# Performance work log

Hardware: AMD Instinct MI355X
Metric: run time of the kernel (lower is better)

## Reference

```python
import jax, jax.numpy as jnp
import numpy as np

N_NODES = 100000
N_EDGES = 600000
DIM = 128
LN_EPS = 1e-5


def setup_inputs() -> dict:
    key = jax.random.key(0)
    ks = jax.random.split(key, 12)
    s = 1.0 / np.sqrt(DIM)
    return {
        "h": jax.random.normal(ks[0], (N_NODES, DIM), dtype=jnp.float32),
        "edge_src": jax.random.randint(ks[1], (N_EDGES,), 0, N_NODES, dtype=jnp.int32),
        "edge_dst": jax.random.randint(ks[2], (N_EDGES,), 0, N_NODES, dtype=jnp.int32),
        "W_self": jax.random.uniform(ks[3], (DIM, DIM), jnp.float32, -s, s),
        "b_self": jax.random.uniform(ks[4], (DIM,), jnp.float32, -s, s),
        "W_neigh": jax.random.uniform(ks[5], (DIM, DIM), jnp.float32, -s, s),
        "b_neigh": jax.random.uniform(ks[6], (DIM,), jnp.float32, -s, s),
        "W_gate": jax.random.uniform(ks[7], (DIM, 2 * DIM), jnp.float32, -s, s),
        "b_gate": jax.random.uniform(ks[8], (DIM,), jnp.float32, -s, s),
        "ln_gamma": jnp.ones((DIM,), jnp.float32),
        "ln_beta": jnp.zeros((DIM,), jnp.float32),
    }


def reference(h, edge_src, edge_dst, W_self, b_self, W_neigh, b_neigh, W_gate, b_gate, ln_gamma, ln_beta):
    n = h.shape[0]
    # self transform: [N, D]
    hs = h @ W_self.T + b_self
    # mean over predecessors via segment sum over edges (src -> dst)
    neigh_sum = jax.ops.segment_sum(h[edge_src], edge_dst, num_segments=n)
    counts = jax.ops.segment_sum(jnp.ones((edge_src.shape[0],), h.dtype), edge_dst, num_segments=n)
    has_pred = (counts > 0).astype(h.dtype)[:, None]
    neigh_mean = neigh_sum / jnp.maximum(counts, 1.0)[:, None]
    hn = neigh_mean @ W_neigh.T + b_neigh
    # nodes with no predecessors skip the neighbor term entirely (incl. bias)
    m = hs + has_pred * hn
    gate = jax.nn.sigmoid(jnp.concatenate([h, m], axis=-1) @ W_gate.T + b_gate)
    v = gate * m + (1.0 - gate) * h
    # LayerNorm (biased variance, as torch) + relu
    mu = jnp.mean(v, axis=-1, keepdims=True)
    var = jnp.mean(jnp.square(v - mu), axis=-1, keepdims=True)
    out = (v - mu) * jax.lax.rsqrt(var + LN_EPS) * ln_gamma + ln_beta
    return jax.nn.relu(out)
```

## Files before the change

### kernel.cpp

```cpp
#include <hip/hip_runtime.h>
#include <math.h>

#define N_NODES 100000
#define N_EDGES 600000
#define DIM 128
#define LN_EPS 1e-5f
#define SCAN_NBLK ((N_NODES + 255) / 256)
#define NTILES ((N_NODES + 127) / 128)
#define NODE_GRID 256

typedef __bf16 bf16x8 __attribute__((ext_vector_type(8)));
typedef __bf16 bf16x4 __attribute__((ext_vector_type(4)));
typedef float f32x4 __attribute__((ext_vector_type(4)));

__global__ __launch_bounds__(256)
void prep_kernel(const float* __restrict__ h, const int* __restrict__ edst,
                 __bf16* __restrict__ h_bf, int* __restrict__ counts) {
  int i = blockIdx.x * 256 + threadIdx.x;
  {
    const float4 v0 = *reinterpret_cast<const float4*>(h + (size_t)i * 8);
    const float4 v1 = *reinterpret_cast<const float4*>(h + (size_t)i * 8 + 4);
    bf16x8 b;
    b[0] = (__bf16)v0.x; b[1] = (__bf16)v0.y; b[2] = (__bf16)v0.z; b[3] = (__bf16)v0.w;
    b[4] = (__bf16)v1.x; b[5] = (__bf16)v1.y; b[6] = (__bf16)v1.z; b[7] = (__bf16)v1.w;
    *reinterpret_cast<bf16x8*>(h_bf + (size_t)i * 8) = b;
  }
  if (i < N_EDGES) atomicAdd(&counts[edst[i]], 1);
}

__global__ __launch_bounds__(256)
void scan1_kernel(const int* __restrict__ counts, int* __restrict__ block_sums) {
  int i = blockIdx.x * 256 + threadIdx.x;
  int v = (i < N_NODES) ? counts[i] : 0;
#pragma unroll
  for (int off = 1; off < 64; off <<= 1) v += __shfl_xor(v, off);
  __shared__ int ws[4];
  if ((threadIdx.x & 63) == 0) ws[threadIdx.x >> 6] = v;
  __syncthreads();
  if (threadIdx.x == 0) block_sums[blockIdx.x] = ws[0] + ws[1] + ws[2] + ws[3];
}

__global__ __launch_bounds__(256)
void scan3_kernel(const int* __restrict__ counts, const int* __restrict__ block_sums,
                  int* __restrict__ row_off, int* __restrict__ cursor) {
  const int i = blockIdx.x * 256 + threadIdx.x;
  const int t = threadIdx.x;
  const int lane = t & 63, wv = t >> 6;
  __shared__ int wtot[4];
  __shared__ int sbase[4];

  int partial = 0;
  for (int j = t; j < blockIdx.x; j += 256) partial += block_sums[j];
#pragma unroll
  for (int off = 1; off < 64; off <<= 1) partial += __shfl_xor(partial, off);
  if (lane == 0) sbase[wv] = partial;
  __syncthreads();
  const int base = sbase[0] + sbase[1] + sbase[2] + sbase[3];

  int v = (i < N_NODES) ? counts[i] : 0;
  int s = v;
#pragma unroll
  for (int off = 1; off < 64; off <<= 1) {
    int u = __shfl_up(s, off);
    if (lane >= off) s += u;
  }
  if (lane == 63) wtot[wv] = s;
  __syncthreads();
  int wo = 0;
  for (int w = 0; w < wv; ++w) wo += wtot[w];
  int excl = base + wo + (s - v);
  if (i < N_NODES) { row_off[i] = excl; cursor[i] = 0; }
  if (i == 0) row_off[N_NODES] = N_EDGES;
}

__global__ __launch_bounds__(256)
void csr_fill_kernel(const int* __restrict__ esrc, const int* __restrict__ edst,
                     const int* __restrict__ row_off, int* __restrict__ cursor,
                     int* __restrict__ csr_src) {
  int base = (blockIdx.x * 256 + threadIdx.x) * 4;
  if (base >= N_EDGES) return;
  int4 s4 = *reinterpret_cast<const int4*>(esrc + base);
  int4 d4 = *reinterpret_cast<const int4*>(edst + base);
  {
    int pos = atomicAdd(&cursor[d4.x], 1);
    csr_src[row_off[d4.x] + pos] = s4.x;
  }
  {
    int pos = atomicAdd(&cursor[d4.y], 1);
    csr_src[row_off[d4.y] + pos] = s4.y;
  }
  {
    int pos = atomicAdd(&cursor[d4.z], 1);
    csr_src[row_off[d4.z] + pos] = s4.z;
  }
  {
    int pos = atomicAdd(&cursor[d4.w], 1);
    csr_src[row_off[d4.w] + pos] = s4.w;
  }
}

__global__ __launch_bounds__(512, 1)
void node_kernel(const __bf16* __restrict__ h_bf,
                 const int* __restrict__ row_off,
                 const int* __restrict__ csr_src,
                 const int* __restrict__ counts,
                 const float* __restrict__ Wself,
                 const float* __restrict__ Wneigh,
                 const float* __restrict__ Wgate,
                 const float* __restrict__ b_self,
                 const float* __restrict__ b_neigh,
                 const float* __restrict__ b_gate,
                 const float* __restrict__ ln_g,
                 const float* __restrict__ ln_b,
                 float* __restrict__ out) {
  __shared__ __align__(16) char smem[163840];
  char* Wl = smem;

  const int tid = threadIdx.x;

  for (int c = tid; c < 8192; c += 512) {
    int mi = c >> 11;
    int w = c & 2047;
    int row = w >> 4, col8 = w & 15;
    const float* src;
    if (mi == 0)      src = Wself  + row * 128 + col8 * 8;
    else if (mi == 1) src = Wneigh + row * 128 + col8 * 8;
    else if (mi == 2) src = Wgate  + row * 256 + col8 * 8;
    else              src = Wgate  + row * 256 + 128 + col8 * 8;
    float4 v0 = *reinterpret_cast<const float4*>(src);
    float4 v1 = *reinterpret_cast<const float4*>(src + 4);
    bf16x8 b;
    b[0] = (__bf16)v0.x; b[1] = (__bf16)v0.y; b[2] = (__bf16)v0.z; b[3] = (__bf16)v0.w;
    b[4] = (__bf16)v1.x; b[5] = (__bf16)v1.y; b[6] = (__bf16)v1.z; b[7] = (__bf16)v1.w;
    int byte = (row * 256 + col8 * 16) ^ ((row & 7) << 4);
    *reinterpret_cast<bf16x8*>(Wl + mi * 32768 + byte) = b;
  }
  __syncthreads();

  const int lane = tid & 63;
  const int wave = tid >> 6;
  const int col = lane & 15;
  const int kb = (lane >> 4) << 3;
  const int rloc = (lane >> 4) << 2;
  char* Ms = smem + 131072 + wave * 4096;

  for (int tile = blockIdx.x; tile < NTILES; tile += NODE_GRID) {
    const int node0 = tile * 128;
    const int n_a = node0 + wave * 16 + col;
    const bool va = n_a < N_NODES;

    bf16x8 a_m[4];
    {
      int b = 0, e = 0;
      if (va) { b = row_off[n_a]; e = row_off[n_a + 1]; }
      float m0[8], m1[8], m2[8], m3[8];
#pragma unroll
      for (int j = 0; j < 8; ++j) { m0[j] = 0.f; m1[j] = 0.f; m2[j] = 0.f; m3[j] = 0.f; }
      int i = b;
      for (; i + 2 <= e; i += 2) {
        int s0 = csr_src[i], s1 = csr_src[i + 1];
        const __bf16* r0 = h_bf + (size_t)s0 * DIM + kb;
        const __bf16* r1 = h_bf + (size_t)s1 * DIM + kb;
        bf16x8 u0 = *reinterpret_cast<const bf16x8*>(r0);
        bf16x8 u1 = *reinterpret_cast<const bf16x8*>(r0 + 32);
        bf16x8 u2 = *reinterpret_cast<const bf16x8*>(r0 + 64);
        bf16x8 u3 = *reinterpret_cast<const bf16x8*>(r0 + 96);
        bf16x8 w0 = *reinterpret_cast<const bf16x8*>(r1);
        bf16x8 w1 = *reinterpret_cast<const bf16x8*>(r1 + 32);
        bf16x8 w2 = *reinterpret_cast<const bf16x8*>(r1 + 64);
        bf16x8 w3 = *reinterpret_cast<const bf16x8*>(r1 + 96);
#pragma unroll
        for (int j = 0; j < 8; ++j) {
          m0[j] += (float)u0[j] + (float)w0[j];
          m1[j] += (float)u1[j] + (float)w1[j];
          m2[j] += (float)u2[j] + (float)w2[j];
          m3[j] += (float)u3[j] + (float)w3[j];
        }
      }
      if (i < e) {
        int s0 = csr_src[i];
        const __bf16* r0 = h_bf + (size_t)s0 * DIM + kb;
        bf16x8 u0 = *reinterpret_cast<const bf16x8*>(r0);
        bf16x8 u1 = *reinterpret_cast<const bf16x8*>(r0 + 32);
        bf16x8 u2 = *reinterpret_cast<const bf16x8*>(r0 + 64);
        bf16x8 u3 = *reinterpret_cast<const bf16x8*>(r0 + 96);
#pragma unroll
        for (int j = 0; j < 8; ++j) {
          m0[j] += (float)u0[j];
          m1[j] += (float)u1[j];
          m2[j] += (float)u2[j];
          m3[j] += (float)u3[j];
        }
      }
      float inv = (e > b) ? 1.0f / (float)(e - b) : 0.0f;
#pragma unroll
      for (int j = 0; j < 8; ++j) {
        a_m[0][j] = (__bf16)(m0[j] * inv);
        a_m[1][j] = (__bf16)(m1[j] * inv);
        a_m[2][j] = (__bf16)(m2[j] * inv);
        a_m[3][j] = (__bf16)(m3[j] * inv);
      }
    }

    bf16x8 a_h[4];
    if (va) {
#pragma unroll
      for (int k0 = 0; k0 < 4; ++k0)
        a_h[k0] = *reinterpret_cast<const bf16x8*>(h_bf + (size_t)n_a * DIM + k0 * 32 + kb);
    } else {
#pragma unroll
      for (int k0 = 0; k0 < 4; ++k0)
#pragma unroll
        for (int j = 0; j < 8; ++j) a_h[k0][j] = (__bf16)0.f;
    }

    int4 c4 = *reinterpret_cast<const int4*>(counts + node0 + wave * 16 + rloc);
    float hp[4];
    {
      int nb0 = node0 + wave * 16 + rloc;
      hp[0] = (nb0 + 0 < N_NODES && c4.x > 0) ? 1.f : 0.f;
      hp[1] = (nb0 + 1 < N_NODES && c4.y > 0) ? 1.f : 0.f;
      hp[2] = (nb0 + 2 < N_NODES && c4.z > 0) ? 1.f : 0.f;
      hp[3] = (nb0 + 3 < N_NODES && c4.w > 0) ? 1.f : 0.f;
    }

    f32x4 sacc[8], nacc[8];
#pragma unroll
    for (int i = 0; i < 8; ++i) {
      sacc[i] = (f32x4){0.f, 0.f, 0.f, 0.f};
      nacc[i] = (f32x4){0.f, 0.f, 0.f, 0.f};
    }
#pragma unroll
    for (int k0 = 0; k0 < 4; ++k0) {
      int koff2 = (k0 * 32 + kb) * 2;
#pragma unroll
      for (int nb = 0; nb < 8; ++nb) {
        int row = nb * 16 + col;
        int swz = (row * 256 + koff2) ^ ((row & 7) << 4);
        bf16x8 bs = *reinterpret_cast<const bf16x8*>(Wl + swz);
        bf16x8 bn = *reinterpret_cast<const bf16x8*>(Wl + 32768 + swz);
        sacc[nb] = __builtin_amdgcn_mfma_f32_16x16x32_bf16(a_h[k0], bs, sacc[nb], 0, 0, 0);
        nacc[nb] = __builtin_amdgcn_mfma_f32_16x16x32_bf16(a_m[k0], bn, nacc[nb], 0, 0, 0);
      }
    }

#pragma unroll
    for (int nb = 0; nb < 8; ++nb) {
      int d = nb * 16 + col;
      float bs = b_self[d], bn = b_neigh[d];
#pragma unroll
      for (int r = 0; r < 4; ++r) {
        float mval = sacc[nb][r] + bs + hp[r] * (nacc[nb][r] + bn);
        sacc[nb][r] = mval;
        int rl = rloc + r;
        int byte = (rl * 256 + d * 2) ^ ((rl & 7) << 4);
        *reinterpret_cast<__bf16*>(Ms + byte) = (__bf16)mval;
      }
    }

    f32x4 gacc[8];
#pragma unroll
    for (int i = 0; i < 8; ++i) gacc[i] = (f32x4){0.f, 0.f, 0.f, 0.f};
#pragma unroll
    for (int k0 = 0; k0 < 4; ++k0) {
      int koff2 = (k0 * 32 + kb) * 2;
      int abyte = (col * 256 + koff2) ^ ((col & 7) << 4);
      bf16x8 am2 = *reinterpret_cast<const bf16x8*>(Ms + abyte);
#pragma unroll
      for (int nb = 0; nb < 8; ++nb) {
        int row = nb * 16 + col;
        int swz = (row * 256 + koff2) ^ ((row & 7) << 4);
        bf16x8 bgh = *reinterpret_cast<const bf16x8*>(Wl + 65536 + swz);
        bf16x8 bgm = *reinterpret_cast<const bf16x8*>(Wl + 98304 + swz);
        gacc[nb] = __builtin_amdgcn_mfma_f32_16x16x32_bf16(a_h[k0], bgh, gacc[nb], 0, 0, 0);
        gacc[nb] = __builtin_amdgcn_mfma_f32_16x16x32_bf16(am2, bgm, gacc[nb], 0, 0, 0);
      }
    }

#pragma unroll
    for (int k0 = 0; k0 < 4; ++k0) {
      int byte = (col * 256 + (k0 * 32 + kb) * 2) ^ ((col & 7) << 4);
      *reinterpret_cast<bf16x8*>(Ms + byte) = a_h[k0];
    }

    float s1[4] = {0.f, 0.f, 0.f, 0.f}, s2[4] = {0.f, 0.f, 0.f, 0.f};
#pragma unroll
    for (int nb = 0; nb < 8; ++nb) {
      int d = nb * 16 + col;
      float bg = b_gate[d];
#pragma unroll
      for (int r = 0; r < 4; ++r) {
        int rl = rloc + r;
        int byte = (rl * 256 + d * 2) ^ ((rl & 7) << 4);
        float hval = (float)*reinterpret_cast<const __bf16*>(Ms + byte);
        float g = 1.0f / (1.0f + __expf(-(gacc[nb][r] + bg)));
        float v = g * sacc[nb][r] + (1.0f - g) * hval;
        s1[r] += v;
        s2[r] += v * v;
        *reinterpret_cast<__bf16*>(Ms + byte) = (__bf16)v;
      }
    }
#pragma unroll
    for (int off = 1; off < 16; off <<= 1) {
#pragma unroll
      for (int r = 0; r < 4; ++r) {
        s1[r] += __shfl_xor(s1[r], off);
        s2[r] += __shfl_xor(s2[r], off);
      }
    }
    float mu[4], rs[4];
#pragma unroll
    for (int r = 0; r < 4; ++r) {
      mu[r] = s1[r] * (1.0f / DIM);
      float var = s2[r] * (1.0f / DIM) - mu[r] * mu[r];
      rs[r] = rsqrtf(var + LN_EPS);
    }

    {
      int orow = lane >> 2;
      int ochunk = lane & 3;
      int gn = node0 + wave * 16 + orow;
      int rsel = orow & 3;
      float muv = (rsel & 2) ? ((rsel & 1) ? mu[3] : mu[2]) : ((rsel & 1) ? mu[1] : mu[0]);
      float rsv = (rsel & 2) ? ((rsel & 1) ? rs[3] : rs[2]) : ((rsel & 1) ? rs[1] : rs[0]);
      bool valid = gn < N_NODES;
#pragma unroll
      for (int j = 0; j < 4; ++j) {
        int d0 = ochunk * 8 + j * 32;
        int byte = (orow * 256 + d0 * 2) ^ ((orow & 7) << 4);
        bf16x8 vb = *reinterpret_cast<const bf16x8*>(Ms + byte);
        float4 g0 = *reinterpret_cast<const float4*>(ln_g + d0);
        float4 g1 = *reinterpret_cast<const float4*>(ln_g + d0 + 4);
        float4 e0 = *reinterpret_cast<const float4*>(ln_b + d0);
        float4 e1 = *reinterpret_cast<const float4*>(ln_b + d0 + 4);
        float4 o0, o1;
        o0.x = fmaxf(((float)vb[0] - muv) * rsv * g0.x + e0.x, 0.f);
        o0.y = fmaxf(((float)vb[1] - muv) * rsv * g0.y + e0.y, 0.f);
        o0.z = fmaxf(((float)vb[2] - muv) * rsv * g0.z + e0.z, 0.f);
        o0.w = fmaxf(((float)vb[3] - muv) * rsv * g0.w + e0.w, 0.f);
        o1.x = fmaxf(((float)vb[4] - muv) * rsv * g1.x + e1.x, 0.f);
        o1.y = fmaxf(((float)vb[5] - muv) * rsv * g1.y + e1.y, 0.f);
        o1.z = fmaxf(((float)vb[6] - muv) * rsv * g1.z + e1.z, 0.f);
        o1.w = fmaxf(((float)vb[7] - muv) * rsv * g1.w + e1.w, 0.f);
        if (valid) {
          *reinterpret_cast<float4*>(out + (size_t)gn * DIM + d0) = o0;
          *reinterpret_cast<float4*>(out + (size_t)gn * DIM + d0 + 4) = o1;
        }
      }
    }
  }
}

extern "C" void kernel_launch(void* const* d_in, const int* in_sizes, int n_in,
                              void* d_out, int out_size, void* d_ws, size_t ws_size,
                              hipStream_t stream) {
  const float* h      = (const float*)d_in[0];
  const int*   esrc   = (const int*)d_in[1];
  const int*   edst   = (const int*)d_in[2];
  const float* Wself  = (const float*)d_in[3];
  const float* bself  = (const float*)d_in[4];
  const float* Wneigh = (const float*)d_in[5];
  const float* bneigh = (const float*)d_in[6];
  const float* Wgate  = (const float*)d_in[7];
  const float* bgate  = (const float*)d_in[8];
  const float* ln_g   = (const float*)d_in[9];
  const float* ln_b   = (const float*)d_in[10];
  float* out = (float*)d_out;

  char* ws = (char*)d_ws;
  int* counts   = (int*)ws;
  int* row_off  = (int*)(ws + 400384);
  int* cursor   = (int*)(ws + 800768);
  int* csr_src  = (int*)(ws + 1200768);
  int* blk_sums = (int*)(ws + 3600768);
  __bf16* h_bf  = (__bf16*)(ws + 3602432);

  hipMemsetAsync(counts, 0, (size_t)N_NODES * sizeof(int), stream);

  prep_kernel<<<6250, 256, 0, stream>>>(h, edst, h_bf, counts);
  scan1_kernel<<<SCAN_NBLK, 256, 0, stream>>>(counts, blk_sums);
  scan3_kernel<<<SCAN_NBLK, 256, 0, stream>>>(counts, blk_sums, row_off, cursor);
  csr_fill_kernel<<<(N_EDGES / 4 + 255) / 256, 256, 0, stream>>>(esrc, edst, row_off, cursor, csr_src);
  node_kernel<<<NODE_GRID, 512, 0, stream>>>(
      h_bf, row_off, csr_src, counts, Wself, Wneigh, Wgate,
      bself, bneigh, bgate, ln_g, ln_b, out);
}
```

Before: 157.4 us.

## Pre-convert weights to bf16 globally and read them from cache instead of LDS

Result: slower. 445.5 us (+183.0%).

```diff
diff --git a/kernel.cpp b/kernel.cpp
--- a/kernel.cpp
+++ b/kernel.cpp
@@ -7,11 +7,34 @@
 #define LN_EPS 1e-5f
 #define SCAN_NBLK ((N_NODES + 255) / 256)
 #define NTILES ((N_NODES + 127) / 128)
-#define NODE_GRID 256
+#define NODE_GRID 512
 
 typedef __bf16 bf16x8 __attribute__((ext_vector_type(8)));
 typedef __bf16 bf16x4 __attribute__((ext_vector_type(4)));
 typedef float f32x4 __attribute__((ext_vector_type(4)));
+
+__global__ __launch_bounds__(256)
+void wconv_kernel(const float* __restrict__ Wself,
+                  const float* __restrict__ Wneigh,
+                  const float* __restrict__ Wgate,
+                  __bf16* __restrict__ wself_bf,
+                  __bf16* __restrict__ wneigh_bf,
+                  __bf16* __restrict__ wgh_bf,
+                  __bf16* __restrict__ wgm_bf) {
+  int i = blockIdx.x * 256 + threadIdx.x;
+  if (i < 16384) {
+    wself_bf[i] = (__bf16)Wself[i];
+  } else if (i < 32768) {
+    int j = i - 16384;
+    wneigh_bf[j] = (__bf16)Wneigh[j];
+  } else {
+    int j = i - 32768;
+    int d = j >> 8, k = j & 255;
+    float v = Wgate[j];
+    if (k < 128) wgh_bf[d * 128 + k] = (__bf16)v;
+    else         wgm_bf[d * 128 + (k - 128)] = (__bf16)v;
+  }
+}
 
 __global__ __launch_bounds__(256)
 void prep_kernel(const float* __restrict__ h, const int* __restrict__ edst,
@@ -104,45 +127,25 @@
                  const int* __restrict__ row_off,
                  const int* __restrict__ csr_src,
                  const int* __restrict__ counts,
-                 const float* __restrict__ Wself,
-                 const float* __restrict__ Wneigh,
-                 const float* __restrict__ Wgate,
+                 const __bf16* __restrict__ wself_bf,
+                 const __bf16* __restrict__ wneigh_bf,
+                 const __bf16* __restrict__ wgh_bf,
+                 const __bf16* __restrict__ wgm_bf,
                  const float* __restrict__ b_self,
                  const float* __restrict__ b_neigh,
                  const float* __restrict__ b_gate,
                  const float* __restrict__ ln_g,
                  const float* __restrict__ ln_b,
                  float* __restrict__ out) {
-  __shared__ __align__(16) char smem[163840];
-  char* Wl = smem;
+  __shared__ __align__(16) char smem[32768];
 
   const int tid = threadIdx.x;
-
-  for (int c = tid; c < 8192; c += 512) {
-    int mi = c >> 11;
-    int w = c & 2047;
-    int row = w >> 4, col8 = w & 15;
-    const float* src;
-    if (mi == 0)      src = Wself  + row * 128 + col8 * 8;
-    else if (mi == 1) src = Wneigh + row * 128 + col8 * 8;
-    else if (mi == 2) src = Wgate  + row * 256 + col8 * 8;
-    else              src = Wgate  + row * 256 + 128 + col8 * 8;
-    float4 v0 = *reinterpret_cast<const float4*>(src);
-    float4 v1 = *reinterpret_cast<const float4*>(src + 4);
-    bf16x8 b;
-    b[0] = (__bf16)v0.x; b[1] = (__bf16)v0.y; b[2] = (__bf16)v0.z; b[3] = (__bf16)v0.w;
-    b[4] = (__bf16)v1.x; b[5] = (__bf16)v1.y; b[6] = (__bf16)v1.z; b[7] = (__bf16)v1.w;
-    int byte = (row * 256 + col8 * 16) ^ ((row & 7) << 4);
-    *reinterpret_cast<bf16x8*>(Wl + mi * 32768 + byte) = b;
-  }
-  __syncthreads();
-
   const int lane = tid & 63;
   const int wave = tid >> 6;
   const int col = lane & 15;
   const int kb = (lane >> 4) << 3;
   const int rloc = (lane >> 4) << 2;
-  char* Ms = smem + 131072 + wave * 4096;
+  char* Ms = smem + wave * 4096;
 
   for (int tile = blockIdx.x; tile < NTILES; tile += NODE_GRID) {
     const int node0 = tile * 128;
@@ -232,13 +235,11 @@
     }
 #pragma unroll
     for (int k0 = 0; k0 < 4; ++k0) {
-      int koff2 = (k0 * 32 + kb) * 2;
 #pragma unroll
       for (int nb = 0; nb < 8; ++nb) {
-        int row = nb * 16 + col;
-        int swz = (row * 256 + koff2) ^ ((row & 7) << 4);
-        bf16x8 bs = *reinterpret_cast<const bf16x8*>(Wl + swz);
-        bf16x8 bn = *reinterpret_cast<const bf16x8*>(Wl + 32768 + swz);
+        int widx = (nb * 16 + col) * 128 + k0 * 32 + kb;
+        bf16x8 bs = *reinterpret_cast<const bf16x8*>(wself_bf + widx);
+        bf16x8 bn = *reinterpret_cast<const bf16x8*>(wneigh_bf + widx);
         sacc[nb] = __builtin_amdgcn_mfma_f32_16x16x32_bf16(a_h[k0], bs, sacc[nb], 0, 0, 0);
         nacc[nb] = __builtin_amdgcn_mfma_f32_16x16x32_bf16(a_m[k0], bn, nacc[nb], 0, 0, 0);
       }
@@ -268,10 +269,9 @@
       bf16x8 am2 = *reinterpret_cast<const bf16x8*>(Ms + abyte);
 #pragma unroll
       for (int nb = 0; nb < 8; ++nb) {
-        int row = nb * 16 + col;
-        int swz = (row * 256 + koff2) ^ ((row & 7) << 4);
-        bf16x8 bgh = *reinterpret_cast<const bf16x8*>(Wl + 65536 + swz);
-        bf16x8 bgm = *reinterpret_cast<const bf16x8*>(Wl + 98304 + swz);
+        int widx = (nb * 16 + col) * 128 + k0 * 32 + kb;
+        bf16x8 bgh = *reinterpret_cast<const bf16x8*>(wgh_bf + widx);
+        bf16x8 bgm = *reinterpret_cast<const bf16x8*>(wgm_bf + widx);
         gacc[nb] = __builtin_amdgcn_mfma_f32_16x16x32_bf16(a_h[k0], bgh, gacc[nb], 0, 0, 0);
         gacc[nb] = __builtin_amdgcn_mfma_f32_16x16x32_bf16(am2, bgm, gacc[nb], 0, 0, 0);
       }
@@ -373,15 +373,21 @@
   int* cursor   = (int*)(ws + 800768);
   int* csr_src  = (int*)(ws + 1200768);
   int* blk_sums = (int*)(ws + 3600768);
-  __bf16* h_bf  = (__bf16*)(ws + 3602432);
+  __bf16* wself_bf  = (__bf16*)(ws + 3602432);
+  __bf16* wneigh_bf = wself_bf + 16384;
+  __bf16* wgh_bf    = wneigh_bf + 16384;
+  __bf16* wgm_bf    = wgh_bf + 16384;
+  __bf16* h_bf      = (__bf16*)(ws + 3733504);
 
   hipMemsetAsync(counts, 0, (size_t)N_NODES * sizeof(int), stream);
 
+  wconv_kernel<<<256, 256, 0, stream>>>(Wself, Wneigh, Wgate,
+                                        wself_bf, wneigh_bf, wgh_bf, wgm_bf);
   prep_kernel<<<6250, 256, 0, stream>>>(h, edst, h_bf, counts);
   scan1_kernel<<<SCAN_NBLK, 256, 0, stream>>>(counts, blk_sums);
   scan3_kernel<<<SCAN_NBLK, 256, 0, stream>>>(counts, blk_sums, row_off, cursor);
   csr_fill_kernel<<<(N_EDGES / 4 + 255) / 256, 256, 0, stream>>>(esrc, edst, row_off, cursor, csr_src);
   node_kernel<<<NODE_GRID, 512, 0, stream>>>(
-      h_bf, row_off, csr_src, counts, Wself, Wneigh, Wgate,
+      h_bf, row_off, csr_src, counts, wself_bf, wneigh_bf, wgh_bf, wgm_bf,
       bself, bneigh, bgate, ln_g, ln_b, out);
 }
```
